# Kernel optimization log

Measured on AMD Instinct MI355X. Metric: run time of the kernel, lower is better.

Reference implementation:

```python
import jax, jax.numpy as jnp
import numpy as np
import math

B, H, S, D = 2, 16, 2048, 64

def setup_inputs() -> dict:
    key = jax.random.key(0)
    kq, kk, kv = jax.random.split(key, 3)
    Q = jax.random.normal(kq, (B, H, S, D), dtype=jnp.float32)
    K = jax.random.normal(kk, (B, H, S, D), dtype=jnp.float32)
    V = jax.random.normal(kv, (B, H, S, D), dtype=jnp.float32)
    causal_mask = jnp.tril(jnp.ones((S, S), dtype=bool))
    return {"Q": Q, "K": K, "V": V, "causal_mask": causal_mask}

def reference(Q, K, V, causal_mask):
    d_k = K.shape[-1]
    scores = jnp.einsum('bhqd,bhkd->bhqk', Q, K) / math.sqrt(d_k)
    scores = jnp.where(causal_mask, scores, -jnp.inf)
    probs = jax.nn.softmax(scores, axis=-1)
    return jnp.einsum('bhqk,bhkd->bhqd', probs, V)
```

## Files before the change

kernel.cpp:

```cpp
#include <hip/hip_runtime.h>
#include <math.h>


constexpr int kS   = 2048;
constexpr int kD   = 64;
constexpr int kBH  = 32;
constexpr int kPadP = 72;

typedef short short8 __attribute__((ext_vector_type(8)));
typedef float float4v __attribute__((ext_vector_type(4)));
typedef float float16v __attribute__((ext_vector_type(16)));
typedef unsigned int u32;
typedef unsigned short u16;

static __device__ inline u16 f2bf(float f) {
  union { float f; unsigned u; } v; v.f = f;
  unsigned r = v.u + 0x7FFF + ((v.u >> 16) & 1);
  return (u16)(r >> 16);
}

static __device__ inline short8 pack8(float4v a, float4v b) {
  short8 r;
  r[0] = (short)f2bf(a[0]); r[1] = (short)f2bf(a[1]);
  r[2] = (short)f2bf(a[2]); r[3] = (short)f2bf(a[3]);
  r[4] = (short)f2bf(b[0]); r[5] = (short)f2bf(b[1]);
  r[6] = (short)f2bf(b[2]); r[7] = (short)f2bf(b[3]);
  return r;
}

static __device__ inline void async_cp16(const void* g, void* l) {
  __builtin_amdgcn_global_load_lds(
      (const __attribute__((address_space(1))) u32*)g,
      (__attribute__((address_space(3))) u32*)l, 16, 0, 0);
}

__global__ __launch_bounds__(256)
void prep_kernel(const float* __restrict__ Q, const float* __restrict__ K,
                 const float* __restrict__ V,
                 u16* __restrict__ Qb, u16* __restrict__ Kb, u16* __restrict__ VT) {
  __shared__ u16 tile[64 * kPadP];
  const int tid = threadIdx.x;
  const int bh = blockIdx.y, st = blockIdx.x;
  const size_t ibase = (size_t)bh * kS * kD + (size_t)st * 64 * kD;
  const int r  = tid >> 2;
  const int c0 = (tid & 3) * 16;
  {
    const float scl = 0.125f * 1.44269504089f;
    const float* qp = Q + ibase + (size_t)r * kD + c0;
    float4v a = *(const float4v*)(qp);
    float4v b = *(const float4v*)(qp + 4);
    float4v c = *(const float4v*)(qp + 8);
    float4v d = *(const float4v*)(qp + 12);
    #pragma unroll
    for (int i = 0; i < 4; ++i) { a[i] *= scl; b[i] *= scl; c[i] *= scl; d[i] *= scl; }
    u16* dst = Qb + ibase + (size_t)r * kD + c0;
    *(short8*)dst       = pack8(a, b);
    *(short8*)(dst + 8) = pack8(c, d);
  }
  {
    const float* kp = K + ibase + (size_t)r * kD + c0;
    float4v a = *(const float4v*)(kp);
    float4v b = *(const float4v*)(kp + 4);
    float4v c = *(const float4v*)(kp + 8);
    float4v d = *(const float4v*)(kp + 12);
    u16* dst = Kb + ibase + (size_t)r * kD + c0;
    *(short8*)dst       = pack8(a, b);
    *(short8*)(dst + 8) = pack8(c, d);
  }
  {
    const float* vp = V + ibase + (size_t)r * kD + c0;
    float4v a = *(const float4v*)(vp);
    float4v b = *(const float4v*)(vp + 4);
    float4v c = *(const float4v*)(vp + 8);
    float4v d = *(const float4v*)(vp + 12);
    u16* t = &tile[r * kPadP + c0];
    *(short8*)t       = pack8(a, b);
    *(short8*)(t + 8) = pack8(c, d);
  }
  __syncthreads();
  {
    const int dd = tid >> 2;
    const int s0 = (tid & 3) * 16;
    short8 w0, w1;
    #pragma unroll
    for (int i = 0; i < 8; ++i) {
      w0[i] = (short)tile[(s0 + i) * kPadP + dd];
      w1[i] = (short)tile[(s0 + 8 + i) * kPadP + dd];
    }
    u16* vdst = VT + (size_t)bh * kD * kS + (size_t)dd * kS + st * 64 + s0;
    *(short8*)vdst       = w0;
    *(short8*)(vdst + 8) = w1;
  }
}

__global__ __launch_bounds__(256, 2)
void fattn_kernel(const u16* __restrict__ Qb, const u16* __restrict__ Kb,
                  const u16* __restrict__ VT,
                  u32* __restrict__ O0, u32* __restrict__ O1,
                  u32* __restrict__ O2, u32* __restrict__ O3,
                  float* __restrict__ Lp) {
  __shared__ __align__(16) u16 ldsK[2][4096];
  __shared__ __align__(16) u16 ldsV[2][4096];

  const int tid  = threadIdx.x;
  const int wave = tid >> 6;
  const int lane = tid & 63;
  const int l31  = lane & 31;
  const int h    = lane >> 5;

  const int bh = blockIdx.y;
  const int p  = blockIdx.x >> 2;
  const int z  = blockIdx.x & 3;
  const int qiA = p, qiB = 7 - p;
  const int nA  = 4 * p + 4;

  const size_t base  = (size_t)bh * kS * kD;
  const size_t vbase = (size_t)bh * kD * kS;

  const int lr  = lane >> 3;
  const int cxl = (lane & 7) ^ lr;
  const int offK0 = lr * 64   + cxl * 8;
  const int offV0 = lr * 2048 + cxl * 8;
  const unsigned hs16 = ((unsigned)(h ^ (l31 & 7))) * 16;

  u32* Od = (z == 0) ? O0 : (z == 1) ? O1 : (z == 2) ? O2 : O3;
  const int cB = 9 * z;
  const int cE = cB + 9;

  short8 ones;
  #pragma unroll
  for (int i = 0; i < 8; ++i) ones[i] = (short)0x3F80;

  int par = 0;
  for (int seg = 0; seg < 2; ++seg) {
    const int qi = seg ? qiB : qiA;
    int tb, te;
    if (seg == 0) { tb = min(cB, nA); te = min(cE, nA); }
    else          { tb = max(cB, nA) - nA; te = max(cE, nA) - nA; }
    const int wq0 = qi * 256 + wave * 64;

    short8 qf[2][4];
    #pragma unroll
    for (int g = 0; g < 2; ++g) {
      const u16* qp = Qb + base + (size_t)(wq0 + 32 * g + l31) * kD + h * 8;
      #pragma unroll
      for (int dk = 0; dk < 4; ++dk) qf[g][dk] = *(const short8*)(qp + dk * 16);
    }

    float16v acc[2][2], lacc[2];
    #pragma unroll
    for (int g = 0; g < 2; ++g) {
      #pragma unroll
      for (int i = 0; i < 16; ++i) { acc[g][0][i] = 0.f; acc[g][1][i] = 0.f; lacc[g][i] = 0.f; }
    }

    if (tb < te) {
      {
        const u16* kg0 = Kb + base + (size_t)tb * 4096;
        const u16* vg0 = VT + vbase + tb * 64;
        const int b = par & 1;
        #pragma unroll
        for (int j = 0; j < 2; ++j) {
          const int g = wave + 4 * j;
          async_cp16(kg0 + g * 512 + offK0,           &ldsK[b][g * 512]);
          async_cp16(vg0 + (size_t)g * 16384 + offV0, &ldsV[b][g * 512]);
        }
      }
      for (int t = tb; t < te; ++t, ++par) {
        __syncthreads();
        if (t + 1 < te) {
          const u16* kg0 = Kb + base + (size_t)(t + 1) * 4096;
          const u16* vg0 = VT + vbase + (t + 1) * 64;
          const int b = (par + 1) & 1;
          #pragma unroll
          for (int j = 0; j < 2; ++j) {
            const int g = wave + 4 * j;
            async_cp16(kg0 + g * 512 + offK0,           &ldsK[b][g * 512]);
            async_cp16(vg0 + (size_t)g * 16384 + offV0, &ldsV[b][g * 512]);
          }
        }
        const char* KB = (const char*)ldsK[par & 1];
        const char* VB = (const char*)ldsV[par & 1];
        #pragma unroll
        for (int kt32 = 0; kt32 < 2; ++kt32) {
          const int ktb = t * 64 + kt32 * 32;
          if (ktb > wq0 + 63) break;

          const char* krow = KB + (kt32 * 32 + l31) * 128;
          short8 kf[4];
          #pragma unroll
          for (int dk = 0; dk < 4; ++dk)
            kf[dk] = *(const short8*)(krow + (((unsigned)(dk * 32)) ^ hs16));
          short8 vf[4];
          #pragma unroll
          for (int c = 0; c < 2; ++c) {
            const unsigned coff = ((unsigned)((kt32 * 4 + 2 * c) * 16)) ^ hs16;
            vf[2 * c]     = *(const short8*)(VB + l31 * 128 + coff);
            vf[2 * c + 1] = *(const short8*)(VB + (32 + l31) * 128 + coff);
          }

          #pragma unroll
          for (int g = 0; g < 2; ++g) {
            if (ktb > wq0 + 32 * g + 31) continue;

            float16v s;
            #pragma unroll
            for (int i = 0; i < 16; ++i) s[i] = 0.f;
            #pragma unroll
            for (int dk = 0; dk < 4; ++dk)
              s = __builtin_amdgcn_mfma_f32_32x32x16_bf16(kf[dk], qf[g][dk], s, 0, 0, 0);

            if (ktb == wq0 + 32 * g) {
              const int qg = wq0 + 32 * g + l31;
              #pragma unroll
              for (int r = 0; r < 16; ++r) {
                const int kg = ktb + (r & 3) + 8 * (r >> 2) + 4 * h;
                if (kg > qg) s[r] = -1e30f;
              }
            }

            u32 pk[8];
            #pragma unroll
            for (int g2 = 0; g2 < 4; ++g2) {
              const u32 u0 = __float_as_uint(__builtin_amdgcn_exp2f(s[4 * g2 + 0]));
              const u32 u1 = __float_as_uint(__builtin_amdgcn_exp2f(s[4 * g2 + 1]));
              const u32 u2 = __float_as_uint(__builtin_amdgcn_exp2f(s[4 * g2 + 2]));
              const u32 u3 = __float_as_uint(__builtin_amdgcn_exp2f(s[4 * g2 + 3]));
              pk[2 * g2]     = __builtin_amdgcn_perm(u1, u0, 0x07060302u);
              pk[2 * g2 + 1] = __builtin_amdgcn_perm(u3, u2, 0x07060302u);
            }
            u32 ek[8];
            #pragma unroll
            for (int i = 0; i < 8; ++i) ek[i] = (u32)__shfl_xor((int)pk[i], 32);

            #pragma unroll
            for (int c = 0; c < 2; ++c) {
              const int ga = 4 * c, gb = 4 * c + 2;
              union { u32 u[4]; short8 s8; } pf;
              pf.u[0] = h ? ek[gb]     : pk[ga];
              pf.u[1] = h ? ek[gb + 1] : pk[ga + 1];
              pf.u[2] = h ? pk[gb]     : ek[ga];
              pf.u[3] = h ? pk[gb + 1] : ek[ga + 1];
              acc[g][0] = __builtin_amdgcn_mfma_f32_32x32x16_bf16(pf.s8, vf[2 * c],     acc[g][0], 0, 0, 0);
              acc[g][1] = __builtin_amdgcn_mfma_f32_32x32x16_bf16(pf.s8, vf[2 * c + 1], acc[g][1], 0, 0, 0);
              lacc[g]   = __builtin_amdgcn_mfma_f32_32x32x16_bf16(pf.s8, ones,          lacc[g],   0, 0, 0);
            }
          }
        }
      }
    }

    #pragma unroll
    for (int g = 0; g < 2; ++g) {
      #pragma unroll
      for (int r = 0; r < 16; ++r) {
        const int row = (r & 3) + 8 * (r >> 2) + 4 * h;
        const u32 w = (u32)f2bf(acc[g][0][r]) | ((u32)f2bf(acc[g][1][r]) << 16);
        Od[((size_t)bh * kS + wq0 + 32 * g + row) * 32 + l31] = w;
      }
      if (l31 == 0) {
        #pragma unroll
        for (int r = 0; r < 16; ++r) {
          const int row = (r & 3) + 8 * (r >> 2) + 4 * h;
          Lp[(size_t)z * kBH * kS + (size_t)bh * kS + wq0 + 32 * g + row] = lacc[g][r];
        }
      }
    }
  }
}

__global__ __launch_bounds__(256)
void combine_kernel(const u32* __restrict__ O0, const u32* __restrict__ O1,
                    const u32* __restrict__ O2, const u32* __restrict__ O3,
                    const float* __restrict__ Lp, float* __restrict__ O) {
  const int idx = blockIdx.x * 256 + threadIdx.x;
  const int row = idx >> 5;
  const int j   = idx & 31;
  const int N = kBH * kS;
  const float l = Lp[row] + Lp[N + row] + Lp[2 * N + row] + Lp[3 * N + row];
  const float inv = 1.f / l;
  const u32 a = O0[idx], b = O1[idx], c = O2[idx], d = O3[idx];
  const float lo = __uint_as_float(a << 16) + __uint_as_float(b << 16)
                 + __uint_as_float(c << 16) + __uint_as_float(d << 16);
  const float hi = __uint_as_float(a & 0xFFFF0000u) + __uint_as_float(b & 0xFFFF0000u)
                 + __uint_as_float(c & 0xFFFF0000u) + __uint_as_float(d & 0xFFFF0000u);
  float* op = O + (size_t)row * kD;
  op[j]      = lo * inv;
  op[j + 32] = hi * inv;
}

extern "C" void kernel_launch(void* const* d_in, const int* in_sizes, int n_in,
                              void* d_out, int out_size, void* d_ws, size_t ws_size,
                              hipStream_t stream) {
  const float* Q = (const float*)d_in[0];
  const float* K = (const float*)d_in[1];
  const float* V = (const float*)d_in[2];
  float* O = (float*)d_out;

  const size_t nKV = (size_t)kBH * kS * kD;
  u16* Qb = (u16*)d_ws;
  u16* Kb = Qb + nKV;
  u16* VT = Kb + nKV;
  u32* O0 = (u32*)(VT + nKV);
  u32* O1 = O0 + nKV / 2;
  u32* O2 = O1 + nKV / 2;
  u32* O3 = O2 + nKV / 2;
  float* Lp = (float*)(O3 + nKV / 2);

  dim3 gprep(kS / 64, kBH);
  prep_kernel<<<gprep, 256, 0, stream>>>(Q, K, V, Qb, Kb, VT);
  dim3 grid(16, kBH);
  fattn_kernel<<<grid, 256, 0, stream>>>(Qb, Kb, VT, O0, O1, O2, O3, Lp);
  combine_kernel<<<(int)(kBH * kS * 32 / 256), 256, 0, stream>>>(O0, O1, O2, O3, Lp, O);
}
```

Baseline: 143.1 us.

## Replace ones-MFMA row sums with VALU sums and permlane32 swaps

The softmax denominator was computed with an extra MFMA against a ones vector. It is now accumulated per lane on the VALU from the bf16-rounded probabilities and combined across the wave halves once at the end. The eight ds_bpermute-based shuffles that exchanged probability halves are replaced with v_permlane32_swap, and s_setprio is raised around the MFMA groups. The aim is to cut a third of the PV-stage MFMA work and the LDS-routed shuffle traffic, at the cost of extra VALU adds per tile.

Result: no change. 142.4 us (-0.5%).

```diff
diff --git a/kernel.cpp b/kernel.cpp
--- a/kernel.cpp
+++ b/kernel.cpp
@@ -32,6 +32,16 @@
   __builtin_amdgcn_global_load_lds(
       (const __attribute__((address_space(1))) u32*)g,
       (__attribute__((address_space(3))) u32*)l, 16, 0, 0);
+}
+
+static __device__ inline void swap32(u32 a, u32 b, u32& oa, u32& ob) {
+#if __has_builtin(__builtin_amdgcn_permlane32_swap)
+  auto r = __builtin_amdgcn_permlane32_swap(a, b, false, false);
+  oa = r[0]; ob = r[1];
+#else
+  asm volatile("v_permlane32_swap_b32 %0, %1" : "+v"(a), "+v"(b));
+  oa = a; ob = b;
+#endif
 }
 
 __global__ __launch_bounds__(256)
@@ -127,9 +137,9 @@
   const int cB = 9 * z;
   const int cE = cB + 9;
 
-  short8 ones;
+  float16v zf;
   #pragma unroll
-  for (int i = 0; i < 8; ++i) ones[i] = (short)0x3F80;
+  for (int i = 0; i < 16; ++i) zf[i] = 0.f;
 
   int par = 0;
   for (int seg = 0; seg < 2; ++seg) {
@@ -147,12 +157,10 @@
       for (int dk = 0; dk < 4; ++dk) qf[g][dk] = *(const short8*)(qp + dk * 16);
     }
 
-    float16v acc[2][2], lacc[2];
-    #pragma unroll
-    for (int g = 0; g < 2; ++g) {
-      #pragma unroll
-      for (int i = 0; i < 16; ++i) { acc[g][0][i] = 0.f; acc[g][1][i] = 0.f; lacc[g][i] = 0.f; }
-    }
+    float16v acc[2][2];
+    float lac[2] = {0.f, 0.f};
+    #pragma unroll
+    for (int g = 0; g < 2; ++g) { acc[g][0] = zf; acc[g][1] = zf; }
 
     if (tb < te) {
       {
@@ -203,12 +211,12 @@
           for (int g = 0; g < 2; ++g) {
             if (ktb > wq0 + 32 * g + 31) continue;
 
-            float16v s;
-            #pragma unroll
-            for (int i = 0; i < 16; ++i) s[i] = 0.f;
-            #pragma unroll
-            for (int dk = 0; dk < 4; ++dk)
-              s = __builtin_amdgcn_mfma_f32_32x32x16_bf16(kf[dk], qf[g][dk], s, 0, 0, 0);
+            __builtin_amdgcn_s_setprio(1);
+            float16v s = __builtin_amdgcn_mfma_f32_32x32x16_bf16(kf[0], qf[g][0], zf, 0, 0, 0);
+            s = __builtin_amdgcn_mfma_f32_32x32x16_bf16(kf[1], qf[g][1], s, 0, 0, 0);
+            s = __builtin_amdgcn_mfma_f32_32x32x16_bf16(kf[2], qf[g][2], s, 0, 0, 0);
+            s = __builtin_amdgcn_mfma_f32_32x32x16_bf16(kf[3], qf[g][3], s, 0, 0, 0);
+            __builtin_amdgcn_s_setprio(0);
 
             if (ktb == wq0 + 32 * g) {
               const int qg = wq0 + 32 * g + l31;
@@ -229,21 +237,28 @@
               pk[2 * g2]     = __builtin_amdgcn_perm(u1, u0, 0x07060302u);
               pk[2 * g2 + 1] = __builtin_amdgcn_perm(u3, u2, 0x07060302u);
             }
-            u32 ek[8];
-            #pragma unroll
-            for (int i = 0; i < 8; ++i) ek[i] = (u32)__shfl_xor((int)pk[i], 32);
+
+            {
+              float e[8];
+              #pragma unroll
+              for (int i = 0; i < 8; ++i)
+                e[i] = __uint_as_float(pk[i] << 16)
+                     + __uint_as_float(pk[i] & 0xFFFF0000u);
+              e[0] += e[1]; e[2] += e[3]; e[4] += e[5]; e[6] += e[7];
+              e[0] += e[2]; e[4] += e[6];
+              lac[g] += e[0] + e[4];
+            }
 
             #pragma unroll
             for (int c = 0; c < 2; ++c) {
               const int ga = 4 * c, gb = 4 * c + 2;
               union { u32 u[4]; short8 s8; } pf;
-              pf.u[0] = h ? ek[gb]     : pk[ga];
-              pf.u[1] = h ? ek[gb + 1] : pk[ga + 1];
-              pf.u[2] = h ? pk[gb]     : ek[ga];
-              pf.u[3] = h ? pk[gb + 1] : ek[ga + 1];
+              swap32(pk[ga],     pk[gb],     pf.u[0], pf.u[2]);
+              swap32(pk[ga + 1], pk[gb + 1], pf.u[1], pf.u[3]);
+              __builtin_amdgcn_s_setprio(1);
               acc[g][0] = __builtin_amdgcn_mfma_f32_32x32x16_bf16(pf.s8, vf[2 * c],     acc[g][0], 0, 0, 0);
               acc[g][1] = __builtin_amdgcn_mfma_f32_32x32x16_bf16(pf.s8, vf[2 * c + 1], acc[g][1], 0, 0, 0);
-              lacc[g]   = __builtin_amdgcn_mfma_f32_32x32x16_bf16(pf.s8, ones,          lacc[g],   0, 0, 0);
+              __builtin_amdgcn_s_setprio(0);
             }
           }
         }
@@ -258,13 +273,9 @@
         const u32 w = (u32)f2bf(acc[g][0][r]) | ((u32)f2bf(acc[g][1][r]) << 16);
         Od[((size_t)bh * kS + wq0 + 32 * g + row) * 32 + l31] = w;
       }
-      if (l31 == 0) {
-        #pragma unroll
-        for (int r = 0; r < 16; ++r) {
-          const int row = (r & 3) + 8 * (r >> 2) + 4 * h;
-          Lp[(size_t)z * kBH * kS + (size_t)bh * kS + wq0 + 32 * g + row] = lacc[g][r];
-        }
-      }
+      const float lt = lac[g] + __shfl_xor(lac[g], 32);
+      if (lane < 32)
+        Lp[(size_t)z * kBH * kS + (size_t)bh * kS + wq0 + 32 * g + lane] = lt;
     }
   }
 }
```
